# Kernel optimization log

Hardware: AMD Instinct MI355X
Metric: run time of the kernel (lower is better)

## Reference

```python
import jax, jax.numpy as jnp
import numpy as np

B, T, I, H = 64, 1024, 512, 512


def setup_inputs() -> dict:
    key = jax.random.key(0)
    ks = jax.random.split(key, 5)
    s = 1.0 / np.sqrt(H)  # PyTorch nn.RNN init scale
    X = jax.random.normal(ks[0], (B, T, I), dtype=jnp.float32)
    W_ih = jax.random.uniform(ks[1], (H, I), minval=-s, maxval=s, dtype=jnp.float32)
    W_hh = jax.random.uniform(ks[2], (H, H), minval=-s, maxval=s, dtype=jnp.float32)
    b_ih = jax.random.uniform(ks[3], (H,), minval=-s, maxval=s, dtype=jnp.float32)
    b_hh = jax.random.uniform(ks[4], (H,), minval=-s, maxval=s, dtype=jnp.float32)
    return {"X": X, "W_ih": W_ih, "W_hh": W_hh, "b_ih": b_ih, "b_hh": b_hh}


def reference(X, W_ih, W_hh, b_ih, b_hh):
    # h_t = tanh(W_ih x_t + b_ih + W_hh h_{t-1} + b_hh)  (PyTorch nn.RNN, tanh)
    # Batch the input-to-hidden GEMM over all timesteps up front.
    Xp = jnp.einsum('bti,hi->bth', X, W_ih) + b_ih + b_hh  # [B,T,H]
    Wt = W_hh.T

    def step(h, xt):
        h = jnp.tanh(xt + h @ Wt)
        return h, h

    h0 = jnp.zeros((X.shape[0], W_hh.shape[0]), dtype=X.dtype)
    _, ys = jax.lax.scan(step, h0, jnp.swapaxes(Xp, 0, 1))  # scan over T
    return jnp.swapaxes(ys, 0, 1)  # [B,T,H]
```

## Files before the change

kernel.cpp:

```cpp
#include <hip/hip_runtime.h>
#include <hip/hip_fp16.h>

typedef unsigned int u32;
typedef _Float16 h2v __attribute__((ext_vector_type(2)));

#define B_ 64
#define T_ 1024
#define H_ 512
#define I_ 512

__device__ __forceinline__ float dot2f(u32 w, u32 h, float acc) {
#if __has_builtin(__builtin_amdgcn_fdot2)
    return __builtin_amdgcn_fdot2(__builtin_bit_cast(h2v, w),
                                  __builtin_bit_cast(h2v, h), acc, false);
#else
    __half2 a = __builtin_bit_cast(__half2, w);
    __half2 b = __builtin_bit_cast(__half2, h);
    return acc + __low2float(a) * __low2float(b) + __high2float(a) * __high2float(b);
#endif
}

__device__ __forceinline__ u32 pkf16(float a, float b) {
    __half2 h = __floats2half2_rn(a, b);
    return __builtin_bit_cast(u32, h);
}

__device__ __forceinline__ float red8(float x) {
    int v = __builtin_bit_cast(int, x);
    x += __builtin_bit_cast(float, __builtin_amdgcn_update_dpp(0, v, 0xB1, 0xF, 0xF, true));
    v = __builtin_bit_cast(int, x);
    x += __builtin_bit_cast(float, __builtin_amdgcn_update_dpp(0, v, 0x4E, 0xF, 0xF, true));
    v = __builtin_bit_cast(int, x);
    x += __builtin_bit_cast(float, __builtin_amdgcn_update_dpp(0, v, 0x141, 0xF, 0xF, true));
    return x;
}

__global__ void prep_w(const float* __restrict__ Whh, u32* __restrict__ wreg,
                       u32* __restrict__ wlds) {
    const int tid = threadIdx.x;
    const int g = tid >> 3, sub = tid & 7;
    const int bid = blockIdx.x;
    if (bid < 208) {
        const int r = bid;
        const int o  = (r < 192) ? (r >> 5) : 6;
        const int k5 = (r < 192) ? (r & 31) : (r - 192);
        const int j = g * 8 + o, i = sub * 64 + 2 * k5;
        wreg[r * 512 + tid] = pkf16(Whh[j * H_ + i], Whh[j * H_ + i + 1]);
    } else {
        const int c = bid - 208;
        int j, cc, half;
        if (c < 4) { cc = 2 + (c >> 1); half = c & 1; j = g * 8 + 6; }
        else       { int c7 = c - 4; cc = c7 >> 1; half = c7 & 1; j = g * 8 + 7; }
        for (int q = 0; q < 4; q++) {
            const int k5 = cc * 8 + half * 4 + q;
            const int i = sub * 64 + 2 * k5;
            wlds[c * 2048 + tid * 4 + q] = pkf16(Whh[j * H_ + i], Whh[j * H_ + i + 1]);
        }
    }
}

#define BM 128
#define BN 64

__launch_bounds__(256, 3)
__global__ void gemm_xp(const float* __restrict__ X, const float* __restrict__ Wih,
                        const float* __restrict__ bih, const float* __restrict__ bhh,
                        float* __restrict__ out) {
    __shared__ u32 Xs[16][BM + 4];
    __shared__ u32 Ws[16][BN + 4];
    const int t = threadIdx.x;
    const int bn = blockIdx.x & 7;
    const int bm = blockIdx.x >> 3;
    const int m0 = bm * BM, n0 = bn * BN;
    const int tm = t & 15, tn = t >> 4;
    float acc[8][4];
#pragma unroll
    for (int i = 0; i < 8; i++)
#pragma unroll
        for (int j = 0; j < 4; j++) acc[i][j] = 0.f;
    const int kc = t & 7, rr = t >> 3;
    const int key = ((tm >> 2) & 1) << 2;
    for (int kt = 0; kt < 16; kt++) {
        const int k0 = kt * 32;
#pragma unroll
        for (int it = 0; it < 4; it++) {
            const int m = it * 32 + rr;
            float4 v = *(const float4*)&X[(size_t)(m0 + m) * I_ + k0 + kc * 4];
            const int mp = m ^ (((m >> 5) & 1) << 2);
            Xs[kc * 2 + 0][mp] = pkf16(v.x, v.y);
            Xs[kc * 2 + 1][mp] = pkf16(v.z, v.w);
        }
#pragma unroll
        for (int it = 0; it < 2; it++) {
            const int n = it * 32 + rr;
            float4 v = *(const float4*)&Wih[(size_t)(n0 + n) * I_ + k0 + kc * 4];
            Ws[kc * 2 + 0][n] = pkf16(v.x, v.y);
            Ws[kc * 2 + 1][n] = pkf16(v.z, v.w);
        }
        __syncthreads();
#pragma unroll
        for (int k2 = 0; k2 < 16; k2++) {
            uint4 a0 = *(const uint4*)&Xs[k2][(tm * 8) ^ key];
            uint4 a1 = *(const uint4*)&Xs[k2][(tm * 8 + 4) ^ key];
            uint4 bv = *(const uint4*)&Ws[k2][tn * 4];
            u32 aa[8] = {a0.x, a0.y, a0.z, a0.w, a1.x, a1.y, a1.z, a1.w};
            u32 bb[4] = {bv.x, bv.y, bv.z, bv.w};
#pragma unroll
            for (int mi = 0; mi < 8; mi++)
#pragma unroll
                for (int ni = 0; ni < 4; ni++)
                    acc[mi][ni] = dot2f(aa[mi], bb[ni], acc[mi][ni]);
        }
        __syncthreads();
    }
    float4 b1 = *(const float4*)&bih[n0 + tn * 4];
    float4 b2 = *(const float4*)&bhh[n0 + tn * 4];
    float4 bs = {b1.x + b2.x, b1.y + b2.y, b1.z + b2.z, b1.w + b2.w};
#pragma unroll
    for (int mi = 0; mi < 8; mi++) {
        const int row = m0 + tm * 8 + mi;
        float4 st = {acc[mi][0] + bs.x, acc[mi][1] + bs.y,
                     acc[mi][2] + bs.z, acc[mi][3] + bs.w};
        *(float4*)&out[(size_t)row * H_ + n0 + tn * 4] = st;
    }
}


#define STEP_K(k, hval)                                         \
    acc0 = dot2f(w2[0 * 32 + cc * 8 + k], (hval), acc0);        \
    acc1 = dot2f(w2[1 * 32 + cc * 8 + k], (hval), acc1);        \
    acc2 = dot2f(w2[2 * 32 + cc * 8 + k], (hval), acc2);        \
    acc3 = dot2f(w2[3 * 32 + cc * 8 + k], (hval), acc3);        \
    acc4 = dot2f(w2[4 * 32 + cc * 8 + k], (hval), acc4);        \
    acc5 = dot2f(w2[5 * 32 + cc * 8 + k], (hval), acc5);

__launch_bounds__(512)
__attribute__((amdgpu_waves_per_eu(2, 2)))
__global__ void rnn_scan(const u32* __restrict__ wreg, const u32* __restrict__ wlds_g,
                         float* __restrict__ out) {
    __shared__ u32 wl[24576];
    __shared__ u32 hh[512];
    const int tid = threadIdx.x;
    const int sub = tid & 7;
    u32 w2[208];
#pragma unroll
    for (int r = 0; r < 208; r++) w2[r] = wreg[r * 512 + tid];
#pragma unroll
    for (int i = 0; i < 48; i++) wl[i * 512 + tid] = wlds_g[i * 512 + tid];
    hh[tid] = 0u;
    __syncthreads();
    float* p = out + (size_t)blockIdx.x * (T_ * H_) + tid;
    const int xorkey = sub << 2;
    __half* hhh = reinterpret_cast<__half*>(hh);
    const int wv = tid >> 1;
    const int wslot = (wv ^ (((wv >> 5) & 7) << 2)) * 2 + (tid & 1);
    const int wbase = tid << 2;
    for (int t = 0; t < T_; t++) {
        const float xp = *p;
        const int rb = (t & 1) << 8;
        float acc0 = 0.f, acc1 = 0.f, acc2 = 0.f, acc3 = 0.f;
        float acc4 = 0.f, acc5 = 0.f, acc6 = 0.f, acc7 = 0.f;
#pragma unroll
        for (int cc = 0; cc < 4; cc++) {
            uint4 hA = *(const uint4*)&hh[rb + ((sub * 32 + cc * 8) ^ xorkey)];
            uint4 hB = *(const uint4*)&hh[rb + ((sub * 32 + cc * 8 + 4) ^ xorkey)];
            uint4 w7a = *(const uint4*)&wl[8192 + (cc * 2 + 0) * 2048 + wbase];
            uint4 w7b = *(const uint4*)&wl[8192 + (cc * 2 + 1) * 2048 + wbase];
            u32 h8[8]  = {hA.x, hA.y, hA.z, hA.w, hB.x, hB.y, hB.z, hB.w};
            u32 w78[8] = {w7a.x, w7a.y, w7a.z, w7a.w, w7b.x, w7b.y, w7b.z, w7b.w};
            u32 w68[8];
            if (cc < 2) {
#pragma unroll
                for (int k = 0; k < 8; k++) w68[k] = w2[192 + cc * 8 + k];
            } else {
                uint4 w6a = *(const uint4*)&wl[((cc - 2) * 2 + 0) * 2048 + wbase];
                uint4 w6b = *(const uint4*)&wl[((cc - 2) * 2 + 1) * 2048 + wbase];
                w68[0] = w6a.x; w68[1] = w6a.y; w68[2] = w6a.z; w68[3] = w6a.w;
                w68[4] = w6b.x; w68[5] = w6b.y; w68[6] = w6b.z; w68[7] = w6b.w;
            }
            STEP_K(0, h8[0]); acc6 = dot2f(w68[0], h8[0], acc6); acc7 = dot2f(w78[0], h8[0], acc7);
            STEP_K(1, h8[1]); acc6 = dot2f(w68[1], h8[1], acc6); acc7 = dot2f(w78[1], h8[1], acc7);
            STEP_K(2, h8[2]); acc6 = dot2f(w68[2], h8[2], acc6); acc7 = dot2f(w78[2], h8[2], acc7);
            STEP_K(3, h8[3]); acc6 = dot2f(w68[3], h8[3], acc6); acc7 = dot2f(w78[3], h8[3], acc7);
            STEP_K(4, h8[4]); acc6 = dot2f(w68[4], h8[4], acc6); acc7 = dot2f(w78[4], h8[4], acc7);
            STEP_K(5, h8[5]); acc6 = dot2f(w68[5], h8[5], acc6); acc7 = dot2f(w78[5], h8[5], acc7);
            STEP_K(6, h8[6]); acc6 = dot2f(w68[6], h8[6], acc6); acc7 = dot2f(w78[6], h8[6], acc7);
            STEP_K(7, h8[7]); acc6 = dot2f(w68[7], h8[7], acc6); acc7 = dot2f(w78[7], h8[7], acc7);
        }
        acc0 = red8(acc0); acc1 = red8(acc1); acc2 = red8(acc2); acc3 = red8(acc3);
        acc4 = red8(acc4); acc5 = red8(acc5); acc6 = red8(acc6); acc7 = red8(acc7);
        float r = acc0;
        if (sub == 1) r = acc1;
        if (sub == 2) r = acc2;
        if (sub == 3) r = acc3;
        if (sub == 4) r = acc4;
        if (sub == 5) r = acc5;
        if (sub == 6) r = acc6;
        if (sub == 7) r = acc7;
        const float pre = xp + r;
        const float e = __expf(-2.f * fabsf(pre));
        const float th = __builtin_copysignf((1.f - e) / (1.f + e), pre);
        *p = th;
        p += H_;
        hhh[(((t & 1) ^ 1) << 9) + wslot] = __float2half(th);
        asm volatile("s_waitcnt lgkmcnt(0)" ::: "memory");
        __builtin_amdgcn_sched_barrier(0);
        __builtin_amdgcn_s_barrier();
        __builtin_amdgcn_sched_barrier(0);
    }
}

extern "C" void kernel_launch(void* const* d_in, const int* in_sizes, int n_in,
                              void* d_out, int out_size, void* d_ws, size_t ws_size,
                              hipStream_t stream) {
    const float* X    = (const float*)d_in[0];
    const float* Wih  = (const float*)d_in[1];
    const float* Whh  = (const float*)d_in[2];
    const float* bih  = (const float*)d_in[3];
    const float* bhh  = (const float*)d_in[4];
    float* out = (float*)d_out;
    u32* wreg = (u32*)d_ws;
    u32* wlds = wreg + 106496;

    prep_w<<<dim3(220), dim3(512), 0, stream>>>(Whh, wreg, wlds);
    gemm_xp<<<dim3((65536 / BM) * (H_ / BN)), dim3(256), 0, stream>>>(X, Wih, bih, bhh, out);
    rnn_scan<<<dim3(B_), dim3(512), 0, stream>>>(wreg, wlds, out);
}
```

Baseline: 1.709 ms.

## Keep row 6 weights in registers and use pairwise-swap butterfly reduction

Moves the whole of output row 6's packed fp16 W_hh slice into registers (224 VGPRs of weights instead of 208), so only row 7 is read from LDS each step and per-step LDS traffic drops. The eight separate 3-stage DPP reductions followed by a select chain are replaced by a butterfly that combines pairs of accumulators at each stage, so each lane ends with its own row's sum after 7 exchanges instead of 24. The h loads are split so the second half is issued after the first four k-steps. The change risks register spills at the 2-waves-per-EU limit, and the last stage uses a cross-row shuffle (__shfl_xor by 4) rather than DPP, which may carry extra latency.

```diff
diff --git a/kernel.cpp b/kernel.cpp
--- a/kernel.cpp
+++ b/kernel.cpp
@@ -25,14 +25,19 @@
     return __builtin_bit_cast(u32, h);
 }
 
-__device__ __forceinline__ float red8(float x) {
-    int v = __builtin_bit_cast(int, x);
-    x += __builtin_bit_cast(float, __builtin_amdgcn_update_dpp(0, v, 0xB1, 0xF, 0xF, true));
-    v = __builtin_bit_cast(int, x);
-    x += __builtin_bit_cast(float, __builtin_amdgcn_update_dpp(0, v, 0x4E, 0xF, 0xF, true));
-    v = __builtin_bit_cast(int, x);
-    x += __builtin_bit_cast(float, __builtin_amdgcn_update_dpp(0, v, 0x141, 0xF, 0xF, true));
-    return x;
+template <int CTRL>
+__device__ __forceinline__ float prs_dpp(float a, float b, bool bit) {
+    float keep = bit ? b : a;
+    float give = bit ? a : b;
+    int gv = __builtin_bit_cast(int, give);
+    float got = __builtin_bit_cast(float,
+        __builtin_amdgcn_update_dpp(0, gv, CTRL, 0xF, 0xF, true));
+    return keep + got;
+}
+__device__ __forceinline__ float prs_shfl4(float a, float b, bool bit) {
+    float keep = bit ? b : a;
+    float give = bit ? a : b;
+    return keep + __shfl_xor(give, 4);
 }
 
 __global__ void prep_w(const float* __restrict__ Whh, u32* __restrict__ wreg,
@@ -40,19 +45,15 @@
     const int tid = threadIdx.x;
     const int g = tid >> 3, sub = tid & 7;
     const int bid = blockIdx.x;
-    if (bid < 208) {
-        const int r = bid;
-        const int o  = (r < 192) ? (r >> 5) : 6;
-        const int k5 = (r < 192) ? (r & 31) : (r - 192);
+    if (bid < 224) {
+        const int r = bid, o = r >> 5, k5 = r & 31;
         const int j = g * 8 + o, i = sub * 64 + 2 * k5;
         wreg[r * 512 + tid] = pkf16(Whh[j * H_ + i], Whh[j * H_ + i + 1]);
     } else {
-        const int c = bid - 208;
-        int j, cc, half;
-        if (c < 4) { cc = 2 + (c >> 1); half = c & 1; j = g * 8 + 6; }
-        else       { int c7 = c - 4; cc = c7 >> 1; half = c7 & 1; j = g * 8 + 7; }
+        const int c = bid - 224;
+        const int j = g * 8 + 7;
         for (int q = 0; q < 4; q++) {
-            const int k5 = cc * 8 + half * 4 + q;
+            const int k5 = c * 4 + q;
             const int i = sub * 64 + 2 * k5;
             wlds[c * 2048 + tid * 4 + q] = pkf16(Whh[j * H_ + i], Whh[j * H_ + i + 1]);
         }
@@ -132,21 +133,22 @@
     acc2 = dot2f(w2[2 * 32 + cc * 8 + k], (hval), acc2);        \
     acc3 = dot2f(w2[3 * 32 + cc * 8 + k], (hval), acc3);        \
     acc4 = dot2f(w2[4 * 32 + cc * 8 + k], (hval), acc4);        \
-    acc5 = dot2f(w2[5 * 32 + cc * 8 + k], (hval), acc5);
+    acc5 = dot2f(w2[5 * 32 + cc * 8 + k], (hval), acc5);        \
+    acc6 = dot2f(w2[6 * 32 + cc * 8 + k], (hval), acc6);
 
 __launch_bounds__(512)
 __attribute__((amdgpu_waves_per_eu(2, 2)))
 __global__ void rnn_scan(const u32* __restrict__ wreg, const u32* __restrict__ wlds_g,
                          float* __restrict__ out) {
-    __shared__ u32 wl[24576];
+    __shared__ u32 wl[16384];
     __shared__ u32 hh[512];
     const int tid = threadIdx.x;
     const int sub = tid & 7;
-    u32 w2[208];
-#pragma unroll
-    for (int r = 0; r < 208; r++) w2[r] = wreg[r * 512 + tid];
-#pragma unroll
-    for (int i = 0; i < 48; i++) wl[i * 512 + tid] = wlds_g[i * 512 + tid];
+    u32 w2[224];
+#pragma unroll
+    for (int r = 0; r < 224; r++) w2[r] = wreg[r * 512 + tid];
+#pragma unroll
+    for (int i = 0; i < 32; i++) wl[i * 512 + tid] = wlds_g[i * 512 + tid];
     hh[tid] = 0u;
     __syncthreads();
     float* p = out + (size_t)blockIdx.x * (T_ * H_) + tid;
@@ -155,6 +157,7 @@
     const int wv = tid >> 1;
     const int wslot = (wv ^ (((wv >> 5) & 7) << 2)) * 2 + (tid & 1);
     const int wbase = tid << 2;
+    const bool b0 = (sub & 1) != 0, b1 = (sub & 2) != 0, b2 = (sub & 4) != 0;
     for (int t = 0; t < T_; t++) {
         const float xp = *p;
         const int rb = (t & 1) << 8;
@@ -163,40 +166,25 @@
 #pragma unroll
         for (int cc = 0; cc < 4; cc++) {
             uint4 hA = *(const uint4*)&hh[rb + ((sub * 32 + cc * 8) ^ xorkey)];
+            uint4 w7a = *(const uint4*)&wl[(cc * 2) * 2048 + wbase];
+            STEP_K(0, hA.x); acc7 = dot2f(w7a.x, hA.x, acc7);
+            STEP_K(1, hA.y); acc7 = dot2f(w7a.y, hA.y, acc7);
+            STEP_K(2, hA.z); acc7 = dot2f(w7a.z, hA.z, acc7);
+            STEP_K(3, hA.w); acc7 = dot2f(w7a.w, hA.w, acc7);
             uint4 hB = *(const uint4*)&hh[rb + ((sub * 32 + cc * 8 + 4) ^ xorkey)];
-            uint4 w7a = *(const uint4*)&wl[8192 + (cc * 2 + 0) * 2048 + wbase];
-            uint4 w7b = *(const uint4*)&wl[8192 + (cc * 2 + 1) * 2048 + wbase];
-            u32 h8[8]  = {hA.x, hA.y, hA.z, hA.w, hB.x, hB.y, hB.z, hB.w};
-            u32 w78[8] = {w7a.x, w7a.y, w7a.z, w7a.w, w7b.x, w7b.y, w7b.z, w7b.w};
-            u32 w68[8];
-            if (cc < 2) {
-#pragma unroll
-                for (int k = 0; k < 8; k++) w68[k] = w2[192 + cc * 8 + k];
-            } else {
-                uint4 w6a = *(const uint4*)&wl[((cc - 2) * 2 + 0) * 2048 + wbase];
-                uint4 w6b = *(const uint4*)&wl[((cc - 2) * 2 + 1) * 2048 + wbase];
-                w68[0] = w6a.x; w68[1] = w6a.y; w68[2] = w6a.z; w68[3] = w6a.w;
-                w68[4] = w6b.x; w68[5] = w6b.y; w68[6] = w6b.z; w68[7] = w6b.w;
-            }
-            STEP_K(0, h8[0]); acc6 = dot2f(w68[0], h8[0], acc6); acc7 = dot2f(w78[0], h8[0], acc7);
-            STEP_K(1, h8[1]); acc6 = dot2f(w68[1], h8[1], acc6); acc7 = dot2f(w78[1], h8[1], acc7);
-            STEP_K(2, h8[2]); acc6 = dot2f(w68[2], h8[2], acc6); acc7 = dot2f(w78[2], h8[2], acc7);
-            STEP_K(3, h8[3]); acc6 = dot2f(w68[3], h8[3], acc6); acc7 = dot2f(w78[3], h8[3], acc7);
-            STEP_K(4, h8[4]); acc6 = dot2f(w68[4], h8[4], acc6); acc7 = dot2f(w78[4], h8[4], acc7);
-            STEP_K(5, h8[5]); acc6 = dot2f(w68[5], h8[5], acc6); acc7 = dot2f(w78[5], h8[5], acc7);
-            STEP_K(6, h8[6]); acc6 = dot2f(w68[6], h8[6], acc6); acc7 = dot2f(w78[6], h8[6], acc7);
-            STEP_K(7, h8[7]); acc6 = dot2f(w68[7], h8[7], acc6); acc7 = dot2f(w78[7], h8[7], acc7);
-        }
-        acc0 = red8(acc0); acc1 = red8(acc1); acc2 = red8(acc2); acc3 = red8(acc3);
-        acc4 = red8(acc4); acc5 = red8(acc5); acc6 = red8(acc6); acc7 = red8(acc7);
-        float r = acc0;
-        if (sub == 1) r = acc1;
-        if (sub == 2) r = acc2;
-        if (sub == 3) r = acc3;
-        if (sub == 4) r = acc4;
-        if (sub == 5) r = acc5;
-        if (sub == 6) r = acc6;
-        if (sub == 7) r = acc7;
+            uint4 w7b = *(const uint4*)&wl[(cc * 2 + 1) * 2048 + wbase];
+            STEP_K(4, hB.x); acc7 = dot2f(w7b.x, hB.x, acc7);
+            STEP_K(5, hB.y); acc7 = dot2f(w7b.y, hB.y, acc7);
+            STEP_K(6, hB.z); acc7 = dot2f(w7b.z, hB.z, acc7);
+            STEP_K(7, hB.w); acc7 = dot2f(w7b.w, hB.w, acc7);
+        }
+        float s0 = prs_dpp<0xB1>(acc0, acc1, b0);
+        float s2 = prs_dpp<0xB1>(acc2, acc3, b0);
+        float s4 = prs_dpp<0xB1>(acc4, acc5, b0);
+        float s6 = prs_dpp<0xB1>(acc6, acc7, b0);
+        float u0 = prs_dpp<0x4E>(s0, s2, b1);
+        float u4 = prs_dpp<0x4E>(s4, s6, b1);
+        float r  = prs_shfl4(u0, u4, b2);
         const float pre = xp + r;
         const float e = __expf(-2.f * fabsf(pre));
         const float th = __builtin_copysignf((1.f - e) / (1.f + e), pre);
@@ -220,9 +208,9 @@
     const float* bhh  = (const float*)d_in[4];
     float* out = (float*)d_out;
     u32* wreg = (u32*)d_ws;
-    u32* wlds = wreg + 106496;
-
-    prep_w<<<dim3(220), dim3(512), 0, stream>>>(Whh, wreg, wlds);
+    u32* wlds = wreg + 114688;
+
+    prep_w<<<dim3(232), dim3(512), 0, stream>>>(Whh, wreg, wlds);
     gemm_xp<<<dim3((65536 / BM) * (H_ / BN)), dim3(256), 0, stream>>>(X, Wih, bih, bhh, out);
     rnn_scan<<<dim3(B_), dim3(512), 0, stream>>>(wreg, wlds, out);
 }
```

Measured after the change: 1.986 ms. 1.16x slower.
